# Optimization experiments

Measured on AMD Instinct MI355X. Metric: run time of the kernel, lower is better.

The kernel has to match this reference:

```python
import jax, jax.numpy as jnp
import numpy as np

N, F, HOPS, HID, NCLS = 100000, 128, 8, 256, 64

def prelu(x, a):
    return jnp.where(x >= 0, x, a * x)

def setup_inputs() -> dict:
    key = jax.random.key(0)
    ks = jax.random.split(key, 8)
    w = lambda i, shape: (jax.random.normal(ks[i], shape, dtype=jnp.float32) * 0.02)
    return {
        "feats": jax.random.normal(ks[0], (HOPS, N, F), dtype=jnp.float32),
        # lr_jk_ref: Dense(HOPS*F, HID) -> PReLU(a_jk) -> Dense(HID, HID)
        "W_jk1": w(1, (HOPS * F, HID)), "b_jk1": jnp.zeros((HID,), jnp.float32),
        "W_jk2": w(2, (HID, HID)),      "b_jk2": jnp.zeros((HID,), jnp.float32),
        # PReLU params (nn.PReLU default init 0.25): FFN-internal, module-level, output-FFN
        "a_jk": jnp.float32(0.25), "a_main": jnp.float32(0.25), "a_out": jnp.float32(0.25),
        # lr_att: Linear(HID + F, 1), split into the jk_ref part and the per-hop x part
        "w_att_ref": w(3, (HID,)), "w_att_x": w(4, (F,)), "b_att": jnp.zeros((), jnp.float32),
        # lr_output: Dense(F, HID) -> PReLU(a_out) -> Dense(HID, NCLS)
        "W_o1": w(5, (F, HID)),  "b_o1": jnp.zeros((HID,), jnp.float32),
        "W_o2": w(6, (HID, NCLS)), "b_o2": jnp.zeros((NCLS,), jnp.float32),
    }

def reference(feats, W_jk1, b_jk1, W_jk2, b_jk2, a_jk, a_main, a_out,
              w_att_ref, w_att_x, b_att, W_o1, b_o1, W_o2, b_o2):
    # feats: [HOPS, N, F]; dropouts are identity (rates = 0 / eval mode)
    n = feats.shape[1]
    # torch.cat(input_list, dim=1) -> [N, HOPS*F]
    concat = jnp.transpose(feats, (1, 0, 2)).reshape(n, -1)
    # lr_jk_ref (FeedForwardNetII, n_layers=2): Dense -> PReLU -> Dense, then module PReLU
    h = prelu(concat @ W_jk1 + b_jk1, a_jk)
    jk_ref = prelu(h @ W_jk2 + b_jk2, a_main)              # [N, HID]
    # attention scores: sigmoid(Linear(cat(jk_ref, x_i))) for each hop i, vectorized
    s_ref = jk_ref @ w_att_ref                              # [N]
    s_x = jnp.einsum('hnf,f->nh', feats, w_att_x)           # [N, HOPS]
    scores = jax.nn.sigmoid(s_x + s_ref[:, None] + b_att)   # [N, HOPS]
    Wsm = jax.nn.softmax(scores, axis=1)                    # softmax over hops
    # weighted multi-hop aggregation: sum_i W[:,i] * x_i
    agg = jnp.einsum('nh,hnf->nf', Wsm, feats)              # [N, F]
    # lr_output (FeedForwardNetII, n_layers=2): Dense -> PReLU -> Dense
    out = prelu(agg @ W_o1 + b_o1, a_out) @ W_o2 + b_o2     # [N, NCLS]
    return out
```

## Files before the change

### kernel.cpp

```cpp
#include <hip/hip_runtime.h>
#include <hip/hip_bf16.h>
#include <cstdint>
#include <cstddef>

#define N_F 128
#define N_HOPS 8
#define N_HID 256
#define N_CLS 64

typedef __bf16 bf16;
typedef __attribute__((ext_vector_type(8))) __bf16 bf16x8;
typedef __attribute__((ext_vector_type(4))) float f32x4;

__device__ inline f32x4 mfma16(bf16x8 a, bf16x8 b, f32x4 c) {
    return __builtin_amdgcn_mfma_f32_16x16x32_bf16(a, b, c, 0, 0, 0);
}

typedef const __attribute__((address_space(1))) unsigned int guint;
typedef __attribute__((address_space(3))) unsigned int luint;
__device__ __forceinline__ void gl_lds16(const void* g, void* l) {
    __builtin_amdgcn_global_load_lds((guint*)g, (luint*)l, 16, 0, 0);
}

__device__ inline void pack_one(const float* __restrict__ s, bf16* __restrict__ d,
                                int NC, int ntn, int idx) {
    const int lane = idx & 63;
    const int f = idx >> 6;
    const int kt = f / ntn, nt = f - kt * ntn;
    const int krow = kt * 32 + ((lane >> 4) << 3);
    const int col = nt * 16 + (lane & 15);
    const float* ss = s + (size_t)krow * NC + col;
    bf16* dd = d + ((size_t)f * 64 + lane) * 8;
#pragma unroll
    for (int j = 0; j < 8; ++j) dd[j] = (bf16)ss[(size_t)j * NC];
}

__global__ void pack_weights(const float* __restrict__ W1, const float* __restrict__ W2,
                             const float* __restrict__ O1, const float* __restrict__ O2,
                             bf16* p1, bf16* p2, bf16* p3, bf16* p4) {
    int i = blockIdx.x * 256 + threadIdx.x;
    if (i < 32768) { pack_one(W1, p1, 256, 16, i); return; }
    i -= 32768;
    if (i < 8192)  { pack_one(W2, p2, 256, 16, i); return; }
    i -= 8192;
    if (i < 4096)  { pack_one(O1, p3, 256, 16, i); return; }
    i -= 4096;
    if (i < 2048)  { pack_one(O2, p4, 64, 4, i); return; }
}

__global__ __launch_bounds__(256) void fused_kernel(
    const float* __restrict__ feats, const bf16* __restrict__ w1p, const bf16* __restrict__ w2p,
    const bf16* __restrict__ o1p, const bf16* __restrict__ o2p,
    const float* __restrict__ b1, const float* __restrict__ b2,
    const float* __restrict__ a_jk_p, const float* __restrict__ a_main_p,
    const float* __restrict__ wref, const float* __restrict__ wax,
    const float* __restrict__ batt_p,
    const float* __restrict__ bo1, const float* __restrict__ a_out_p,
    const float* __restrict__ bo2, float* __restrict__ out, int N)
{
    union __align__(16) U {
        bf16 B[2][8192];
        bf16 H[64 * 264];
        bf16 AG[64 * 136];
        bf16 HO[64 * 264];
    };
    __shared__ U u;
    __shared__ float sx[64 * 8];
    __shared__ float sref[64];

    const int t = threadIdx.x;
    const int lane = t & 63;
    const int wv = t >> 6;
    const int row0 = blockIdx.x * 64;
    const int rA = lane & 15;
    const int cA = lane >> 4;

    if (t < 64) sref[t] = 0.f;

    const int growA = min(row0 + (wv << 4) + rA, N - 1);
    const float* arow = feats + (size_t)growA * N_F + (cA << 3);
    const size_t hopstride = (size_t)N * N_F;

    f32x4 acc[16] = {};
    float pacc = 0.f;

    float4 v0 = *(const float4*)(arow);
    float4 v1 = *(const float4*)(arow + 4);
#pragma unroll
    for (int q = 0; q < 4; ++q)
        gl_lds16(w1p + q * 2048 + t * 8, &u.B[0][q * 2048 + t * 8]);
    __syncthreads();

#pragma unroll 2
    for (int kt = 0; kt < 32; ++kt) {
        const int cur = kt & 1;
        float4 v0n, v1n;
        if (kt < 31) {
            const int kn = kt + 1;
            const float* np = arow + (size_t)(kn >> 2) * hopstride + ((kn & 3) << 5);
            v0n = *(const float4*)np;
            v1n = *(const float4*)(np + 4);
            const bf16* bsrc = w1p + (size_t)kn * 8192;
#pragma unroll
            for (int q = 0; q < 4; ++q)
                gl_lds16(bsrc + q * 2048 + t * 8, &u.B[cur ^ 1][q * 2048 + t * 8]);
        }
        const int f0 = ((kt & 3) << 5) + (cA << 3);
        const float4 wx0 = *(const float4*)&wax[f0];
        const float4 wx1 = *(const float4*)&wax[f0 + 4];
        pacc += v0.x * wx0.x + v0.y * wx0.y + v0.z * wx0.z + v0.w * wx0.w
              + v1.x * wx1.x + v1.y * wx1.y + v1.z * wx1.z + v1.w * wx1.w;
        if ((kt & 3) == 3) {
            pacc += __shfl_xor(pacc, 16, 64);
            pacc += __shfl_xor(pacc, 32, 64);
            if (lane < 16) sx[(((wv << 4) + lane) << 3) + (kt >> 2)] = pacc;
            pacc = 0.f;
        }
        bf16x8 af;
        af[0] = (bf16)v0.x; af[1] = (bf16)v0.y; af[2] = (bf16)v0.z; af[3] = (bf16)v0.w;
        af[4] = (bf16)v1.x; af[5] = (bf16)v1.y; af[6] = (bf16)v1.z; af[7] = (bf16)v1.w;
#pragma unroll
        for (int j = 0; j < 16; ++j) {
            const bf16x8 bfr = *(const bf16x8*)&u.B[cur][((j << 6) + lane) << 3];
            acc[j] = mfma16(af, bfr, acc[j]);
        }
        if (kt < 31) { v0 = v0n; v1 = v1n; }
        __syncthreads();
    }

    const float ajk = *a_jk_p;
#pragma unroll
    for (int j = 0; j < 16; ++j) {
        const int colg = (j << 4) + rA;
        const float bias = b1[colg];
#pragma unroll
        for (int r = 0; r < 4; ++r) {
            const int row = (wv << 4) + (cA << 2) + r;
            float v = acc[j][r] + bias;
            v = v >= 0.f ? v : ajk * v;
            u.H[row * 264 + colg] = (bf16)v;
        }
    }
    __syncthreads();

    f32x4 acc2[4][4] = {};
    for (int kt = 0; kt < 8; ++kt) {
        bf16x8 af2[4], bfr[4];
#pragma unroll
        for (int i = 0; i < 4; ++i)
            af2[i] = *(bf16x8*)&u.H[((i << 4) + rA) * 264 + (kt << 5) + (cA << 3)];
#pragma unroll
        for (int j = 0; j < 4; ++j)
            bfr[j] = *(const bf16x8*)&w2p[((size_t)((kt << 4) + (wv << 2) + j) * 64 + lane) * 8];
#pragma unroll
        for (int i = 0; i < 4; ++i)
#pragma unroll
            for (int j = 0; j < 4; ++j)
                acc2[i][j] = mfma16(af2[i], bfr[j], acc2[i][j]);
    }

    const float amain = *a_main_p;
    float pr[4][4] = {};
#pragma unroll
    for (int j = 0; j < 4; ++j) {
        const int colg = (wv << 6) + (j << 4) + rA;
        const float bias = b2[colg];
        const float wr_ = wref[colg];
#pragma unroll
        for (int i = 0; i < 4; ++i)
#pragma unroll
            for (int r = 0; r < 4; ++r) {
                float v = acc2[i][j][r] + bias;
                v = v >= 0.f ? v : amain * v;
                pr[i][r] += v * wr_;
            }
    }
#pragma unroll
    for (int m = 1; m < 16; m <<= 1)
#pragma unroll
        for (int i = 0; i < 4; ++i)
#pragma unroll
            for (int r = 0; r < 4; ++r)
                pr[i][r] += __shfl_xor(pr[i][r], m, 64);
    if (rA == 0) {
#pragma unroll
        for (int i = 0; i < 4; ++i)
#pragma unroll
            for (int r = 0; r < 4; ++r)
                atomicAdd(&sref[(i << 4) + (cA << 2) + r], pr[i][r]);
    }
    __syncthreads();

    if (t < 64) {
        const float srf = sref[t] + *batt_p;
        float e[8], mx = -1e30f;
#pragma unroll
        for (int h = 0; h < 8; ++h) {
            const float s = 1.f / (1.f + expf(-(sx[(t << 3) + h] + srf)));
            e[h] = s; mx = fmaxf(mx, s);
        }
        float sum = 0.f;
#pragma unroll
        for (int h = 0; h < 8; ++h) { e[h] = expf(e[h] - mx); sum += e[h]; }
        const float inv = 1.f / sum;
#pragma unroll
        for (int h = 0; h < 8; ++h) sx[(t << 3) + h] = e[h] * inv;
    }
    __syncthreads();

    {
        const int r = t >> 2;
        const int c = t & 3;
        const int rg = min(row0 + r, N - 1);
        const float* bp = feats + (size_t)rg * N_F + (c << 5);
        f32x4 a4[8] = {};
        f32x4 pA[8], pB[8];
#pragma unroll
        for (int q = 0; q < 8; ++q) pA[q] = ((const f32x4*)bp)[q];
#pragma unroll
        for (int h = 0; h < 8; ++h) {
            if (h < 7) {
                const f32x4* np = (const f32x4*)(bp + hopstride * (h + 1));
#pragma unroll
                for (int q = 0; q < 8; ++q) pB[q] = np[q];
            }
            const float wgt = sx[(r << 3) + h];
#pragma unroll
            for (int q = 0; q < 8; ++q) a4[q] += wgt * pA[q];
            if (h < 7) {
#pragma unroll
                for (int q = 0; q < 8; ++q) pA[q] = pB[q];
            }
        }
#pragma unroll
        for (int q2 = 0; q2 < 4; ++q2) {
            bf16x8 av;
#pragma unroll
            for (int e2 = 0; e2 < 4; ++e2) {
                av[e2] = (bf16)a4[q2 * 2][e2];
                av[4 + e2] = (bf16)a4[q2 * 2 + 1][e2];
            }
            *(bf16x8*)&u.AG[r * 136 + (c << 5) + q2 * 8] = av;
        }
    }
    __syncthreads();

    f32x4 acc3[4][4] = {};
    for (int kt = 0; kt < 4; ++kt) {
        bf16x8 af3[4], bfr[4];
#pragma unroll
        for (int i = 0; i < 4; ++i)
            af3[i] = *(bf16x8*)&u.AG[((i << 4) + rA) * 136 + (kt << 5) + (cA << 3)];
#pragma unroll
        for (int j = 0; j < 4; ++j)
            bfr[j] = *(const bf16x8*)&o1p[((size_t)((kt << 4) + (wv << 2) + j) * 64 + lane) * 8];
#pragma unroll
        for (int i = 0; i < 4; ++i)
#pragma unroll
            for (int j = 0; j < 4; ++j)
                acc3[i][j] = mfma16(af3[i], bfr[j], acc3[i][j]);
    }
    __syncthreads();

    const float aout = *a_out_p;
#pragma unroll
    for (int j = 0; j < 4; ++j) {
        const int colg = (wv << 6) + (j << 4) + rA;
        const float bias = bo1[colg];
#pragma unroll
        for (int i = 0; i < 4; ++i)
#pragma unroll
            for (int r = 0; r < 4; ++r) {
                const int row = (i << 4) + (cA << 2) + r;
                float v = acc3[i][j][r] + bias;
                v = v >= 0.f ? v : aout * v;
                u.HO[row * 264 + colg] = (bf16)v;
            }
    }
    __syncthreads();

    f32x4 acc4[4] = {};
    for (int kt = 0; kt < 8; ++kt) {
        const bf16x8 b = *(const bf16x8*)&o2p[((size_t)((kt << 2) + wv) * 64 + lane) * 8];
#pragma unroll
        for (int i = 0; i < 4; ++i) {
            const bf16x8 a = *(bf16x8*)&u.HO[((i << 4) + rA) * 264 + (kt << 5) + (cA << 3)];
            acc4[i] = mfma16(a, b, acc4[i]);
        }
    }
    {
        const int colg = (wv << 4) + rA;
        const float bv = bo2[colg];
#pragma unroll
        for (int i = 0; i < 4; ++i)
#pragma unroll
            for (int r = 0; r < 4; ++r) {
                const int rg = row0 + (i << 4) + (cA << 2) + r;
                if (rg < N) out[(size_t)rg * 64 + colg] = acc4[i][r] + bv;
            }
    }
}

extern "C" void kernel_launch(void* const* d_in, const int* in_sizes, int n_in,
                              void* d_out, int out_size, void* d_ws, size_t ws_size,
                              hipStream_t stream) {
    const float* feats  = (const float*)d_in[0];
    const float* W1     = (const float*)d_in[1];
    const float* b1     = (const float*)d_in[2];
    const float* W2     = (const float*)d_in[3];
    const float* b2     = (const float*)d_in[4];
    const float* a_jk   = (const float*)d_in[5];
    const float* a_main = (const float*)d_in[6];
    const float* a_out  = (const float*)d_in[7];
    const float* wref   = (const float*)d_in[8];
    const float* wax    = (const float*)d_in[9];
    const float* batt   = (const float*)d_in[10];
    const float* O1     = (const float*)d_in[11];
    const float* bo1    = (const float*)d_in[12];
    const float* O2     = (const float*)d_in[13];
    const float* bo2    = (const float*)d_in[14];

    const int N = in_sizes[0] / (N_HOPS * N_F);

    char* ws = (char*)d_ws;
    bf16* p1 = (bf16*)ws;
    bf16* p2 = (bf16*)(ws + 524288);
    bf16* p3 = (bf16*)(ws + 655360);
    bf16* p4 = (bf16*)(ws + 720896);

    pack_weights<<<184, 256, 0, stream>>>(W1, W2, O1, O2, p1, p2, p3, p4);
    const int nb = (N + 63) / 64;
    fused_kernel<<<nb, 256, 0, stream>>>(feats, p1, p2, p3, p4, b1, b2,
                                         a_jk, a_main, wref, wax, batt,
                                         bo1, a_out, bo2, (float*)d_out, N);
}
```

Measured before the change: 722.8 us.

## Deepen first-GEMM pipeline to two-stage prefetch with manual waitcnt barriers

Restructures the main K loop so feature rows are prefetched two iterations ahead through a 3-slot register ring, and weight tiles are loaded into LDS two stages ahead. Each iteration waits on a specific vmcnt before a raw s_barrier instead of calling __syncthreads. It also stages w_att_x in LDS, fully unrolls the later GEMM loops, and adds a minimum-occupancy hint to launch_bounds. The goal is to hide global-memory latency behind MFMA work. In exchange, register pressure rises and the hand-counted waitcnt values must exactly match the number of outstanding loads.

Result: slower. 758.2 us (+4.9%).

```diff
diff --git a/kernel.cpp b/kernel.cpp
--- a/kernel.cpp
+++ b/kernel.cpp
@@ -48,7 +48,7 @@
     if (i < 2048)  { pack_one(O2, p4, 64, 4, i); return; }
 }
 
-__global__ __launch_bounds__(256) void fused_kernel(
+__global__ __launch_bounds__(256, 4) void fused_kernel(
     const float* __restrict__ feats, const bf16* __restrict__ w1p, const bf16* __restrict__ w2p,
     const bf16* __restrict__ o1p, const bf16* __restrict__ o2p,
     const float* __restrict__ b1, const float* __restrict__ b2,
@@ -67,6 +67,7 @@
     __shared__ U u;
     __shared__ float sx[64 * 8];
     __shared__ float sref[64];
+    __shared__ float waxl[128];
 
     const int t = threadIdx.x;
     const int lane = t & 63;
@@ -76,6 +77,7 @@
     const int cA = lane >> 4;
 
     if (t < 64) sref[t] = 0.f;
+    if (t < 128) waxl[t] = wax[t];
 
     const int growA = min(row0 + (wv << 4) + rA, N - 1);
     const float* arow = feats + (size_t)growA * N_F + (cA << 3);
@@ -84,30 +86,40 @@
     f32x4 acc[16] = {};
     float pacc = 0.f;
 
-    float4 v0 = *(const float4*)(arow);
-    float4 v1 = *(const float4*)(arow + 4);
+    float4 bA[3][2];
+    bA[0][0] = *(const float4*)(arow);
+    bA[0][1] = *(const float4*)(arow + 4);
+    bA[1][0] = *(const float4*)(arow + 32);
+    bA[1][1] = *(const float4*)(arow + 36);
 #pragma unroll
     for (int q = 0; q < 4; ++q)
         gl_lds16(w1p + q * 2048 + t * 8, &u.B[0][q * 2048 + t * 8]);
-    __syncthreads();
-
-#pragma unroll 2
+#pragma unroll
+    for (int q = 0; q < 4; ++q)
+        gl_lds16(w1p + 8192 + q * 2048 + t * 8, &u.B[1][q * 2048 + t * 8]);
+
+#pragma unroll
     for (int kt = 0; kt < 32; ++kt) {
         const int cur = kt & 1;
-        float4 v0n, v1n;
-        if (kt < 31) {
-            const int kn = kt + 1;
+        __builtin_amdgcn_sched_barrier(0);
+        if (kt == 0)       asm volatile("s_waitcnt vmcnt(4)" ::: "memory");
+        else if (kt == 31) asm volatile("s_waitcnt vmcnt(0)" ::: "memory");
+        else               asm volatile("s_waitcnt vmcnt(6)" ::: "memory");
+        __builtin_amdgcn_s_barrier();
+        __builtin_amdgcn_sched_barrier(0);
+
+        if (kt + 2 < 32) {
+            const int kn = kt + 2;
             const float* np = arow + (size_t)(kn >> 2) * hopstride + ((kn & 3) << 5);
-            v0n = *(const float4*)np;
-            v1n = *(const float4*)(np + 4);
-            const bf16* bsrc = w1p + (size_t)kn * 8192;
-#pragma unroll
-            for (int q = 0; q < 4; ++q)
-                gl_lds16(bsrc + q * 2048 + t * 8, &u.B[cur ^ 1][q * 2048 + t * 8]);
-        }
+            bA[(kt + 2) % 3][0] = *(const float4*)np;
+            bA[(kt + 2) % 3][1] = *(const float4*)(np + 4);
+        }
+
+        const float4 v0 = bA[kt % 3][0];
+        const float4 v1 = bA[kt % 3][1];
         const int f0 = ((kt & 3) << 5) + (cA << 3);
-        const float4 wx0 = *(const float4*)&wax[f0];
-        const float4 wx1 = *(const float4*)&wax[f0 + 4];
+        const float4 wx0 = *(const float4*)&waxl[f0];
+        const float4 wx1 = *(const float4*)&waxl[f0 + 4];
         pacc += v0.x * wx0.x + v0.y * wx0.y + v0.z * wx0.z + v0.w * wx0.w
               + v1.x * wx1.x + v1.y * wx1.y + v1.z * wx1.z + v1.w * wx1.w;
         if ((kt & 3) == 3) {
@@ -116,6 +128,7 @@
             if (lane < 16) sx[(((wv << 4) + lane) << 3) + (kt >> 2)] = pacc;
             pacc = 0.f;
         }
+
         bf16x8 af;
         af[0] = (bf16)v0.x; af[1] = (bf16)v0.y; af[2] = (bf16)v0.z; af[3] = (bf16)v0.w;
         af[4] = (bf16)v1.x; af[5] = (bf16)v1.y; af[6] = (bf16)v1.z; af[7] = (bf16)v1.w;
@@ -124,8 +137,16 @@
             const bf16x8 bfr = *(const bf16x8*)&u.B[cur][((j << 6) + lane) << 3];
             acc[j] = mfma16(af, bfr, acc[j]);
         }
-        if (kt < 31) { v0 = v0n; v1 = v1n; }
-        __syncthreads();
+
+        __builtin_amdgcn_sched_barrier(0);
+        __builtin_amdgcn_s_barrier();
+        __builtin_amdgcn_sched_barrier(0);
+        if (kt + 2 < 32) {
+            const bf16* bsrc = w1p + (size_t)(kt + 2) * 8192;
+#pragma unroll
+            for (int q = 0; q < 4; ++q)
+                gl_lds16(bsrc + q * 2048 + t * 8, &u.B[cur][q * 2048 + t * 8]);
+        }
     }
 
     const float ajk = *a_jk_p;
@@ -144,6 +165,7 @@
     __syncthreads();
 
     f32x4 acc2[4][4] = {};
+#pragma unroll
     for (int kt = 0; kt < 8; ++kt) {
         bf16x8 af2[4], bfr[4];
 #pragma unroll
@@ -246,6 +268,7 @@
     __syncthreads();
 
     f32x4 acc3[4][4] = {};
+#pragma unroll
     for (int kt = 0; kt < 4; ++kt) {
         bf16x8 af3[4], bfr[4];
 #pragma unroll
@@ -280,6 +303,7 @@
     __syncthreads();
 
     f32x4 acc4[4] = {};
+#pragma unroll
     for (int kt = 0; kt < 8; ++kt) {
         const bf16x8 b = *(const bf16x8*)&o2p[((size_t)((kt << 2) + wv) * 64 + lane) * 8];
 #pragma unroll
```
